# Optimization experiments

Measured on AMD Instinct MI355X. Metric: run time of the kernel, lower is better.

## Reference

```python
import jax, jax.numpy as jnp
import numpy as np

N = 50000      # nodes
E = 800000     # edges (before self-loops)
F_IN = 256
H = 4          # heads
C1 = 128
C2 = 64
NCLS = 50
NEG_SLOPE = 0.2


def setup_inputs() -> dict:
    key = jax.random.key(0)
    ks = jax.random.split(key, 12)
    x = jax.random.normal(ks[0], (N, F_IN), dtype=jnp.float32)
    edge_index = jax.random.randint(ks[1], (2, E), 0, N, dtype=jnp.int32)
    s1 = 1.0 / np.sqrt(F_IN)
    s2 = 1.0 / np.sqrt(H * C1)
    s3 = 1.0 / np.sqrt(H * C2)
    return {
        "x": x,
        "edge_index": edge_index,
        "W1": jax.random.normal(ks[2], (F_IN, H * C1), dtype=jnp.float32) * s1,
        "a_src1": jax.random.normal(ks[3], (H, C1), dtype=jnp.float32) * s2,
        "a_dst1": jax.random.normal(ks[4], (H, C1), dtype=jnp.float32) * s2,
        "b1": jnp.zeros((H * C1,), dtype=jnp.float32),
        "W2": jax.random.normal(ks[5], (H * C1, H * C2), dtype=jnp.float32) * s2,
        "a_src2": jax.random.normal(ks[6], (H, C2), dtype=jnp.float32) * s3,
        "a_dst2": jax.random.normal(ks[7], (H, C2), dtype=jnp.float32) * s3,
        "b2": jnp.zeros((H * C2,), dtype=jnp.float32),
        "Wf": jax.random.normal(ks[8], (H * C2, NCLS), dtype=jnp.float32) * s3,
        "bf": jnp.zeros((NCLS,), dtype=jnp.float32),
    }


def _gat_conv(x, src, dst, W, a_src, a_dst, b, heads, ch):
    # h: [N, H, C] transformed features
    h = (x @ W).reshape(N, heads, ch)
    # per-node attention halves (standard GAT decomposition, avoids per-edge d-dim gather for scores)
    asrc = jnp.sum(h * a_src[None], axis=-1)  # [N, H]
    adst = jnp.sum(h * a_dst[None], axis=-1)  # [N, H]
    e = jax.nn.leaky_relu(asrc[src] + adst[dst], NEG_SLOPE)  # [E, H]
    # softmax over edges sharing the same destination node
    m = jax.ops.segment_max(e, dst, num_segments=N)          # [N, H]
    ex = jnp.exp(e - m[dst])
    denom = jax.ops.segment_sum(ex, dst, num_segments=N)     # [N, H]
    alpha = ex / (denom[dst] + 1e-16)                        # [E, H]
    msg = h[src] * alpha[:, :, None]                         # [E, H, C]
    out = jax.ops.segment_sum(msg, dst, num_segments=N)      # [N, H, C]
    return out.reshape(N, heads * ch) + b


def reference(x, edge_index, W1, a_src1, a_dst1, b1, W2, a_src2, a_dst2, b2, Wf, bf):
    # PyG GATConv adds self-loops by default
    loops = jnp.arange(N, dtype=edge_index.dtype)
    src = jnp.concatenate([edge_index[0], loops])
    dst = jnp.concatenate([edge_index[1], loops])
    h = _gat_conv(x, src, dst, W1, a_src1, a_dst1, b1, H, C1)
    h = jax.nn.elu(h)
    # F.dropout is identity in eval mode
    h = _gat_conv(h, src, dst, W2, a_src2, a_dst2, b2, H, C2)
    h = jax.nn.elu(h)
    return h @ Wf + bf
```

## Files before the change

kernel.cpp:

```cpp
#include <hip/hip_runtime.h>
#include <hip/hip_fp16.h>
#include <cmath>

#define NN 50000
#define EE 800000
#define ET 850000
#define HH 4
#define CC1 128
#define CC2 64
#define FIN 256
#define NCLS 50

typedef _Float16 half8_t __attribute__((ext_vector_type(8)));
typedef __attribute__((ext_vector_type(4))) float floatx4;

typedef const __attribute__((address_space(1))) unsigned int* glds_gp_t;
typedef __attribute__((address_space(3))) unsigned int* glds_lp_t;
__device__ __forceinline__ void glds16(const void* g, void* l) {
    __builtin_amdgcn_global_load_lds((glds_gp_t)g, (glds_lp_t)l, 16, 0, 0);
}

#define NB_CAST 12500
#define NB_W1   512
#define NB_W2   512
#define NB_WF   64
__global__ __launch_bounds__(256) void prep_fused(
    const float* __restrict__ x, __half* __restrict__ xb,
    const float* __restrict__ W1, __half* __restrict__ W1t,
    const float* __restrict__ W2, __half* __restrict__ W2t,
    const float* __restrict__ Wf, __half* __restrict__ Wft)
{
    int b = blockIdx.x;
    if (b < NB_CAST) {
        int t = b * 256 + threadIdx.x;
        float4 v = *(const float4*)(x + 4 * (size_t)t);
        __half2 p[2];
        p[0] = __floats2half2_rn(v.x, v.y);
        p[1] = __floats2half2_rn(v.z, v.w);
        *(uint2*)(xb + 4 * (size_t)t) = *(uint2*)p;
    } else if (b < NB_CAST + NB_W1) {
        int t = (b - NB_CAST) * 256 + threadIdx.x;
        int n = t >> 8, k = t & 255;
        W1t[t] = __float2half(W1[(size_t)k * 512 + n]);
    } else if (b < NB_CAST + NB_W1 + NB_W2) {
        int t = (b - NB_CAST - NB_W1) * 256 + threadIdx.x;
        int n = t >> 9, k = t & 511;
        W2t[t] = __float2half(W2[(size_t)k * 256 + n]);
    } else {
        int t = (b - NB_CAST - NB_W1 - NB_W2) * 256 + threadIdx.x;
        int n = t >> 8, k = t & 255;
        Wft[t] = (n < NCLS) ? __float2half(Wf[(size_t)k * NCLS + n]) : __float2half(0.f);
    }
}

__global__ __launch_bounds__(256) void gemm_f16_v2(
    const __half* __restrict__ A,
    const __half* __restrict__ Bt,
    __half* __restrict__ C,
    int M, int N, int K)
{
    __shared__ __half As[128 * 32];
    __shared__ __half Bs[128 * 32];
    int tid = threadIdx.x, wave = tid >> 6, lane = tid & 63;
    int wm = (wave >> 1) * 64, wn = (wave & 1) * 64;
    int row0 = blockIdx.x * 128, col0 = blockIdx.y * 128;
    int lm = lane & 15, lq = lane >> 4, kq = lq * 8;
    floatx4 acc[4][4] = {};

    int srow = wave * 32 + (lane >> 2);
    int skk  = (lane & 3) * 8;
    int gra0 = row0 + srow;      if (gra0 >= M) gra0 = M - 1;
    int gra1 = row0 + srow + 16; if (gra1 >= M) gra1 = M - 1;
    const __half* ga0 = A + (size_t)gra0 * K + skk;
    const __half* ga1 = A + (size_t)gra1 * K + skk;
    const __half* gb0 = Bt + (size_t)(col0 + srow) * K + skk;
    const __half* gb1 = Bt + (size_t)(col0 + srow + 16) * K + skk;
    __half* la0 = &As[(wave * 32) * 32];
    __half* la1 = &As[(wave * 32 + 16) * 32];
    __half* lb0 = &Bs[(wave * 32) * 32];
    __half* lb1 = &Bs[(wave * 32 + 16) * 32];

    for (int k0 = 0; k0 < K; k0 += 32) {
        __syncthreads();
        glds16(ga0 + k0, la0);
        glds16(ga1 + k0, la1);
        glds16(gb0 + k0, lb0);
        glds16(gb1 + k0, lb1);
        __syncthreads();

        half8_t af[4], bfr[4];
        #pragma unroll
        for (int mt = 0; mt < 4; ++mt)
            af[mt] = *(const half8_t*)&As[(wm + mt * 16 + lm) * 32 + kq];
        #pragma unroll
        for (int nt = 0; nt < 4; ++nt)
            bfr[nt] = *(const half8_t*)&Bs[(wn + nt * 16 + lm) * 32 + kq];
        #pragma unroll
        for (int mt = 0; mt < 4; ++mt)
            #pragma unroll
            for (int nt = 0; nt < 4; ++nt)
                acc[mt][nt] = __builtin_amdgcn_mfma_f32_16x16x32_f16(
                    af[mt], bfr[nt], acc[mt][nt], 0, 0, 0);
    }

    #pragma unroll
    for (int mt = 0; mt < 4; ++mt) {
        int rbase = row0 + wm + mt * 16 + lq * 4;
        #pragma unroll
        for (int nt = 0; nt < 4; ++nt) {
            int c = col0 + wn + nt * 16 + lm;
            #pragma unroll
            for (int r = 0; r < 4; ++r) {
                int gr = rbase + r;
                if (gr < M) C[(size_t)gr * N + c] = __float2half(acc[mt][nt][r]);
            }
        }
    }
}

__global__ __launch_bounds__(128) void gemm_final(
    const __half* __restrict__ A,
    const __half* __restrict__ Bt,
    const float* __restrict__ bias,
    float* __restrict__ out, int M)
{
    __shared__ __half As[128 * 40];
    __shared__ __half Bs[64 * 40];
    int tid = threadIdx.x, wave = tid >> 6, lane = tid & 63;
    int row0 = blockIdx.x * 128;
    int lm = lane & 15, lq = lane >> 4, kq = lq * 8;
    floatx4 acc[4][4] = {};

    for (int k0 = 0; k0 < 256; k0 += 32) {
        int gr = row0 + tid; if (gr >= M) gr = M - 1;
        const __half* ap = A + (size_t)gr * 256 + k0;
        half8_t a0 = *(const half8_t*)ap;
        half8_t a1 = *(const half8_t*)(ap + 8);
        half8_t a2 = *(const half8_t*)(ap + 16);
        half8_t a3 = *(const half8_t*)(ap + 24);
        const __half* bp = Bt + (size_t)(tid >> 1) * 256 + k0 + (tid & 1) * 16;
        half8_t b0 = *(const half8_t*)bp;
        half8_t b1 = *(const half8_t*)(bp + 8);
        __syncthreads();
        *(half8_t*)&As[tid * 40 + 0]  = a0;
        *(half8_t*)&As[tid * 40 + 8]  = a1;
        *(half8_t*)&As[tid * 40 + 16] = a2;
        *(half8_t*)&As[tid * 40 + 24] = a3;
        *(half8_t*)&Bs[(tid >> 1) * 40 + (tid & 1) * 16]     = b0;
        *(half8_t*)&Bs[(tid >> 1) * 40 + (tid & 1) * 16 + 8] = b1;
        __syncthreads();

        half8_t af[4], bfr[4];
        #pragma unroll
        for (int mt = 0; mt < 4; ++mt)
            af[mt] = *(const half8_t*)&As[(wave * 64 + mt * 16 + lm) * 40 + kq];
        #pragma unroll
        for (int nt = 0; nt < 4; ++nt)
            bfr[nt] = *(const half8_t*)&Bs[(nt * 16 + lm) * 40 + kq];
        #pragma unroll
        for (int mt = 0; mt < 4; ++mt)
            #pragma unroll
            for (int nt = 0; nt < 4; ++nt)
                acc[mt][nt] = __builtin_amdgcn_mfma_f32_16x16x32_f16(
                    af[mt], bfr[nt], acc[mt][nt], 0, 0, 0);
    }

    #pragma unroll
    for (int mt = 0; mt < 4; ++mt) {
        int rbase = row0 + wave * 64 + mt * 16 + lq * 4;
        #pragma unroll
        for (int nt = 0; nt < 4; ++nt) {
            int c = nt * 16 + lm;
            if (c >= NCLS) continue;
            float bv = bias[c];
            #pragma unroll
            for (int r = 0; r < 4; ++r) {
                int gr = rbase + r;
                if (gr < M) out[(size_t)gr * NCLS + c] = acc[mt][nt][r] + bv;
            }
        }
    }
}

template<int C>
__global__ __launch_bounds__(256) void attn_scores2(
    const __half* __restrict__ h, const float* __restrict__ a_src,
    const float* __restrict__ a_dst, float* __restrict__ asrc,
    float* __restrict__ adst)
{
    constexpr int HC = HH * C;
    constexpr int CPL = HC / 64;
    int wave = threadIdx.x >> 6;
    int lane = threadIdx.x & 63;
    int n = blockIdx.x * 4 + wave;
    if (n >= NN) return;
    int c0 = lane * CPL;
    int head = c0 / C;
    const __half* hp = h + (size_t)n * HC + c0;
    float hv[CPL];
    if (CPL == 8) {
        union { uint4 u; __half2 h2[4]; } U;
        U.u = *(const uint4*)hp;
        #pragma unroll
        for (int k = 0; k < 4; ++k) {
            float2 f = __half22float2(U.h2[k]);
            hv[2 * k] = f.x; hv[2 * k + 1] = f.y;
        }
    } else {
        union { uint2 u; __half2 h2[2]; } U;
        U.u = *(const uint2*)hp;
        #pragma unroll
        for (int k = 0; k < 2; ++k) {
            float2 f = __half22float2(U.h2[k]);
            hv[2 * k] = f.x; hv[2 * k + 1] = f.y;
        }
    }
    float s1 = 0.f, s2 = 0.f;
    #pragma unroll
    for (int c = 0; c < CPL; ++c) {
        s1 += hv[c] * a_src[c0 + c];
        s2 += hv[c] * a_dst[c0 + c];
    }
    #pragma unroll
    for (int o = 8; o > 0; o >>= 1) {
        s1 += __shfl_xor(s1, o, 64);
        s2 += __shfl_xor(s2, o, 64);
    }
    if ((lane & 15) == 0) {
        asrc[n * HH + head] = s1;
        adst[n * HH + head] = s2;
    }
}

__global__ void edge_histogram(const int* __restrict__ ei, int* __restrict__ deg)
{
    int t = blockIdx.x * blockDim.x + threadIdx.x;
    if (t >= ET) return;
    int dst = (t < EE) ? ei[EE + t] : (t - EE);
    atomicAdd(&deg[dst], 1);
}

__global__ __launch_bounds__(256) void scan_reduce(
    const int* __restrict__ deg, int* __restrict__ partials)
{
    int i0 = blockIdx.x * 2048 + threadIdx.x * 8;
    int s = 0;
    #pragma unroll
    for (int k = 0; k < 8; ++k) { int i = i0 + k; s += (i < NN) ? deg[i] : 0; }
    #pragma unroll
    for (int o = 32; o > 0; o >>= 1) s += __shfl_xor(s, o, 64);
    __shared__ int ws[4];
    int lane = threadIdx.x & 63, wid = threadIdx.x >> 6;
    if (lane == 0) ws[wid] = s;
    __syncthreads();
    if (threadIdx.x == 0) partials[blockIdx.x] = ws[0] + ws[1] + ws[2] + ws[3];
}

#define SCAN_NB 25
__global__ __launch_bounds__(256) void scan_apply(
    const int* __restrict__ deg, const int* __restrict__ partials,
    int* __restrict__ off, int* __restrict__ pos)
{
    __shared__ int spE[SCAN_NB];
    __shared__ int ws[4];
    int lane = threadIdx.x & 63, wid = threadIdx.x >> 6;
    if (wid == 0) {
        int v = (lane < SCAN_NB) ? partials[lane] : 0;
        int s = v;
        #pragma unroll
        for (int o = 1; o < 32; o <<= 1) {
            int t = __shfl_up(s, o, 64);
            if (lane >= o) s += t;
        }
        if (lane < SCAN_NB) spE[lane] = s - v;
    }

    int i0 = blockIdx.x * 2048 + threadIdx.x * 8;
    int v[8]; int s = 0;
    #pragma unroll
    for (int k = 0; k < 8; ++k) {
        int i = i0 + k;
        v[k] = (i < NN) ? deg[i] : 0;
        s += v[k];
    }
    int sc = s;
    #pragma unroll
    for (int o = 1; o < 64; o <<= 1) {
        int t = __shfl_up(sc, o, 64);
        if (lane >= o) sc += t;
    }
    if (lane == 63) ws[wid] = sc;
    __syncthreads();
    int woff = spE[blockIdx.x];
    for (int w = 0; w < wid; ++w) woff += ws[w];
    int excl = woff + sc - s;
    #pragma unroll
    for (int k = 0; k < 8; ++k) {
        int i = i0 + k;
        if (i < NN) { off[i] = excl; pos[i] = excl; }
        excl += v[k];
    }
    if (blockIdx.x == 0 && threadIdx.x == 0) off[NN] = ET;
}

__global__ void edge_scatter(const int* __restrict__ ei,
                             int* __restrict__ pos, int* __restrict__ csr_src)
{
    int t = blockIdx.x * blockDim.x + threadIdx.x;
    if (t >= ET) return;
    int src, dst;
    if (t < EE) { src = ei[t]; dst = ei[EE + t]; }
    else        { src = t - EE; dst = t - EE; }
    int p = atomicAdd(&pos[dst], 1);
    csr_src[p] = src;
}

template<int C>
__global__ __launch_bounds__(256) void aggregate7(
    const __half* __restrict__ h, const int* __restrict__ off,
    const int* __restrict__ csr_src, const float* __restrict__ asrc,
    const float* __restrict__ adst, const float* __restrict__ bias,
    __half* __restrict__ outb)
{
    constexpr int HC = HH * C;
    constexpr int LPE = HC / 8;
    constexpr int EPW = 64 / LPE;
    constexpr int UNR = 8;
    __shared__ unsigned int exlds_all[4][64 * HH];
    int wave = threadIdx.x >> 6;
    int lane = threadIdx.x & 63;
    int n = blockIdx.x * 4 + wave;
    if (n >= NN) return;
    unsigned int* exlds = exlds_all[wave];
    int el  = (EPW == 1) ? 0 : (lane >> 5);
    int lel = (EPW == 1) ? lane : (lane & 31);
    int coff = lel * 8;
    int hl = coff / C;

    int start = off[n], end = off[n + 1];
    float4 advv = *(const float4*)(adst + (size_t)n * HH);
    float dh0 = 0.f, dh1 = 0.f, dh2 = 0.f, dh3 = 0.f;
    __half2 acc2[4] = {};

    for (int cb = start; cb < end; cb += 64) {
        int eidx = cb + lane;
        bool valid = eidx < end;
        int s_lane = csr_src[valid ? eidx : end - 1];
        float4 t = *(const float4*)(asrc + (size_t)s_lane * HH);
        float e0 = t.x + advv.x; e0 = e0 > 0.f ? e0 : 0.2f * e0;
        float e1 = t.y + advv.y; e1 = e1 > 0.f ? e1 : 0.2f * e1;
        float e2 = t.z + advv.z; e2 = e2 > 0.f ? e2 : 0.2f * e2;
        float e3 = t.w + advv.w; e3 = e3 > 0.f ? e3 : 0.2f * e3;
        float x0 = valid ? __expf(e0) : 0.f;
        float x1 = valid ? __expf(e1) : 0.f;
        float x2 = valid ? __expf(e2) : 0.f;
        float x3 = valid ? __expf(e3) : 0.f;
        dh0 += x0; dh1 += x1; dh2 += x2; dh3 += x3;
        __half2 xp[4];
        xp[0] = __float2half2_rn(x0);
        xp[1] = __float2half2_rn(x1);
        xp[2] = __float2half2_rn(x2);
        xp[3] = __float2half2_rn(x3);
        *(uint4*)&exlds[lane * 4] = *(uint4*)xp;

        int cnt = end - cb; if (cnt > 64) cnt = 64;
        int jmax = (cnt + UNR * EPW - 1) & ~(UNR * EPW - 1);
        for (int jj = 0; jj < jmax; jj += UNR * EPW) {
            int sidx[UNR]; __half2 xs[UNR];
            union { uint4 u; __half2 h2[4]; } uv[UNR];
            #pragma unroll
            for (int u = 0; u < UNR; ++u) {
                int e_lo = jj + u * EPW;
                if (EPW == 1) {
                    sidx[u] = __builtin_amdgcn_readlane(s_lane, e_lo);
                } else {
                    int sa = __builtin_amdgcn_readlane(s_lane, e_lo);
                    int sb = __builtin_amdgcn_readlane(s_lane, e_lo + 1);
                    sidx[u] = el ? sb : sa;
                }
                uv[u].u = *(const uint4*)(h + (size_t)sidx[u] * HC + coff);
                xs[u] = *(__half2*)&exlds[(e_lo + el) * 4 + hl];
            }
            #pragma unroll
            for (int u = 0; u < UNR; ++u)
                #pragma unroll
                for (int k = 0; k < 4; ++k)
                    acc2[k] = __hfma2(xs[u], uv[u].h2[k], acc2[k]);
        }
    }

    #pragma unroll
    for (int o = 32; o > 0; o >>= 1) {
        dh0 += __shfl_xor(dh0, o, 64);
        dh1 += __shfl_xor(dh1, o, 64);
        dh2 += __shfl_xor(dh2, o, 64);
        dh3 += __shfl_xor(dh3, o, 64);
    }
    float accf[8];
    #pragma unroll
    for (int k = 0; k < 4; ++k) {
        float2 f = __half22float2(acc2[k]);
        accf[2 * k] = f.x; accf[2 * k + 1] = f.y;
    }
    if (EPW == 2) {
        #pragma unroll
        for (int c = 0; c < 8; ++c)
            accf[c] += __shfl_xor(accf[c], 32, 64);
    }
    float d = (hl == 0) ? dh0 : (hl == 1) ? dh1 : (hl == 2) ? dh2 : dh3;
    float inv = 1.f / (d + 1e-16f);
    if (el == 0) {
        float4 b0 = *(const float4*)(bias + coff);
        float4 b1 = *(const float4*)(bias + coff + 4);
        float bb[8] = {b0.x, b0.y, b0.z, b0.w, b1.x, b1.y, b1.z, b1.w};
        __half2 pk[4];
        #pragma unroll
        for (int c2 = 0; c2 < 4; ++c2) {
            float ua = accf[2 * c2]     * inv + bb[2 * c2];
            float ub = accf[2 * c2 + 1] * inv + bb[2 * c2 + 1];
            ua = ua > 0.f ? ua : expm1f(ua);
            ub = ub > 0.f ? ub : expm1f(ub);
            pk[c2] = __floats2half2_rn(ua, ub);
        }
        *(uint4*)(outb + (size_t)n * HC + coff) = *(uint4*)pk;
    }
}

extern "C" void kernel_launch(void* const* d_in, const int* in_sizes, int n_in,
                              void* d_out, int out_size, void* d_ws, size_t ws_size,
                              hipStream_t stream) {
    const float* x      = (const float*)d_in[0];
    const int*   ei     = (const int*)d_in[1];
    const float* W1     = (const float*)d_in[2];
    const float* a_src1 = (const float*)d_in[3];
    const float* a_dst1 = (const float*)d_in[4];
    const float* b1     = (const float*)d_in[5];
    const float* W2     = (const float*)d_in[6];
    const float* a_src2 = (const float*)d_in[7];
    const float* a_dst2 = (const float*)d_in[8];
    const float* b2     = (const float*)d_in[9];
    const float* Wf     = (const float*)d_in[10];
    const float* bf     = (const float*)d_in[11];
    float* out = (float*)d_out;

    char* p = (char*)d_ws;
    __half* xb    = (__half*)p; p += (size_t)NN * FIN * 2;
    __half* h1b   = (__half*)p; p += (size_t)NN * HH * CC1 * 2;
    __half* out1b = (__half*)p; p += (size_t)NN * HH * CC1 * 2;
    __half* h2b   = (__half*)p; p += (size_t)NN * HH * CC2 * 2;
    __half* out2b = (__half*)p; p += (size_t)NN * HH * CC2 * 2;
    __half* W1t   = (__half*)p; p += (size_t)FIN * HH * CC1 * 2;
    __half* W2t   = (__half*)p; p += (size_t)HH * CC1 * HH * CC2 * 2;
    __half* Wft   = (__half*)p; p += (size_t)64 * HH * CC2 * 2;
    float* asrc   = (float*)p;  p += (size_t)NN * HH * 4;
    float* adst   = (float*)p;  p += (size_t)NN * HH * 4;
    int* deg      = (int*)p;    p += (size_t)NN * 4;
    int* csr_off  = (int*)p;    p += (size_t)(NN + 1) * 4 + 12;
    int* csr_pos  = (int*)p;    p += (size_t)NN * 4;
    int* csr_src  = (int*)p;    p += (size_t)ET * 4;
    int* partials = (int*)p;    p += 64 * 4;

    hipMemsetAsync(deg, 0, NN * sizeof(int), stream);

    prep_fused<<<NB_CAST + NB_W1 + NB_W2 + NB_WF, 256, 0, stream>>>(
        x, xb, W1, W1t, W2, W2t, Wf, Wft);

    edge_histogram<<<(ET + 255) / 256, 256, 0, stream>>>(ei, deg);
    scan_reduce<<<SCAN_NB, 256, 0, stream>>>(deg, partials);
    scan_apply<<<SCAN_NB, 256, 0, stream>>>(deg, partials, csr_off, csr_pos);
    edge_scatter<<<(ET + 255) / 256, 256, 0, stream>>>(ei, csr_pos, csr_src);

    gemm_f16_v2<<<dim3((NN + 127) / 128, (HH * CC1) / 128), 256, 0, stream>>>(
        xb, W1t, h1b, NN, HH * CC1, FIN);
    attn_scores2<CC1><<<(NN + 3) / 4, 256, 0, stream>>>(h1b, a_src1, a_dst1, asrc, adst);
    aggregate7<CC1><<<(NN + 3) / 4, 256, 0, stream>>>(h1b, csr_off, csr_src, asrc, adst, b1, out1b);

    gemm_f16_v2<<<dim3((NN + 127) / 128, (HH * CC2) / 128), 256, 0, stream>>>(
        out1b, W2t, h2b, NN, HH * CC2, HH * CC1);
    attn_scores2<CC2><<<(NN + 3) / 4, 256, 0, stream>>>(h2b, a_src2, a_dst2, asrc, adst);
    aggregate7<CC2><<<(NN + 3) / 4, 256, 0, stream>>>(h2b, csr_off, csr_src, asrc, adst, b2, out2b);

    gemm_final<<<(NN + 127) / 128, 128, 0, stream>>>(out2b, Wft, bf, out, NN);
}
```

Before: 498.5 us.

## Fuse histogram into prep kernel, merge scan passes, grid-stride attention/aggregate

```diff
diff --git a/kernel.cpp b/kernel.cpp
--- a/kernel.cpp
+++ b/kernel.cpp
@@ -24,11 +24,13 @@
 #define NB_W1   512
 #define NB_W2   512
 #define NB_WF   64
-__global__ __launch_bounds__(256) void prep_fused(
+#define NB_HIST 3321
+__global__ __launch_bounds__(256) void prep_hist(
     const float* __restrict__ x, __half* __restrict__ xb,
     const float* __restrict__ W1, __half* __restrict__ W1t,
     const float* __restrict__ W2, __half* __restrict__ W2t,
-    const float* __restrict__ Wf, __half* __restrict__ Wft)
+    const float* __restrict__ Wf, __half* __restrict__ Wft,
+    const int* __restrict__ ei, int* __restrict__ deg)
 {
     int b = blockIdx.x;
     if (b < NB_CAST) {
@@ -46,10 +48,16 @@
         int t = (b - NB_CAST - NB_W1) * 256 + threadIdx.x;
         int n = t >> 9, k = t & 511;
         W2t[t] = __float2half(W2[(size_t)k * 256 + n]);
-    } else {
+    } else if (b < NB_CAST + NB_W1 + NB_W2 + NB_WF) {
         int t = (b - NB_CAST - NB_W1 - NB_W2) * 256 + threadIdx.x;
         int n = t >> 8, k = t & 255;
         Wft[t] = (n < NCLS) ? __float2half(Wf[(size_t)k * NCLS + n]) : __float2half(0.f);
+    } else {
+        int t = (b - NB_CAST - NB_W1 - NB_W2 - NB_WF) * 256 + threadIdx.x;
+        if (t < ET) {
+            int dst = (t < EE) ? ei[EE + t] : (t - EE);
+            atomicAdd(&deg[dst], 1);
+        }
     }
 }
 
@@ -183,99 +191,79 @@
 }
 
 template<int C>
-__global__ __launch_bounds__(256) void attn_scores2(
+__global__ __launch_bounds__(256) void attn_scores3(
     const __half* __restrict__ h, const float* __restrict__ a_src,
     const float* __restrict__ a_dst, float* __restrict__ asrc,
-    float* __restrict__ adst)
+    float* __restrict__ adst, int nwaves)
 {
     constexpr int HC = HH * C;
     constexpr int CPL = HC / 64;
     int wave = threadIdx.x >> 6;
     int lane = threadIdx.x & 63;
-    int n = blockIdx.x * 4 + wave;
-    if (n >= NN) return;
+    int wid0 = blockIdx.x * 4 + wave;
     int c0 = lane * CPL;
     int head = c0 / C;
-    const __half* hp = h + (size_t)n * HC + c0;
-    float hv[CPL];
-    if (CPL == 8) {
-        union { uint4 u; __half2 h2[4]; } U;
-        U.u = *(const uint4*)hp;
-        #pragma unroll
-        for (int k = 0; k < 4; ++k) {
-            float2 f = __half22float2(U.h2[k]);
-            hv[2 * k] = f.x; hv[2 * k + 1] = f.y;
-        }
-    } else {
-        union { uint2 u; __half2 h2[2]; } U;
-        U.u = *(const uint2*)hp;
-        #pragma unroll
-        for (int k = 0; k < 2; ++k) {
-            float2 f = __half22float2(U.h2[k]);
-            hv[2 * k] = f.x; hv[2 * k + 1] = f.y;
-        }
-    }
-    float s1 = 0.f, s2 = 0.f;
-    #pragma unroll
-    for (int c = 0; c < CPL; ++c) {
-        s1 += hv[c] * a_src[c0 + c];
-        s2 += hv[c] * a_dst[c0 + c];
-    }
-    #pragma unroll
-    for (int o = 8; o > 0; o >>= 1) {
-        s1 += __shfl_xor(s1, o, 64);
-        s2 += __shfl_xor(s2, o, 64);
-    }
-    if ((lane & 15) == 0) {
-        asrc[n * HH + head] = s1;
-        adst[n * HH + head] = s2;
-    }
-}
-
-__global__ void edge_histogram(const int* __restrict__ ei, int* __restrict__ deg)
-{
-    int t = blockIdx.x * blockDim.x + threadIdx.x;
-    if (t >= ET) return;
-    int dst = (t < EE) ? ei[EE + t] : (t - EE);
-    atomicAdd(&deg[dst], 1);
-}
-
-__global__ __launch_bounds__(256) void scan_reduce(
-    const int* __restrict__ deg, int* __restrict__ partials)
-{
-    int i0 = blockIdx.x * 2048 + threadIdx.x * 8;
-    int s = 0;
-    #pragma unroll
-    for (int k = 0; k < 8; ++k) { int i = i0 + k; s += (i < NN) ? deg[i] : 0; }
-    #pragma unroll
-    for (int o = 32; o > 0; o >>= 1) s += __shfl_xor(s, o, 64);
+
+    for (int n = wid0; n < NN; n += nwaves) {
+        const __half* hp = h + (size_t)n * HC + c0;
+        float hv[CPL];
+        if (CPL == 8) {
+            union { uint4 u; __half2 h2[4]; } U;
+            U.u = *(const uint4*)hp;
+            #pragma unroll
+            for (int k = 0; k < 4; ++k) {
+                float2 f = __half22float2(U.h2[k]);
+                hv[2 * k] = f.x; hv[2 * k + 1] = f.y;
+            }
+        } else {
+            union { uint2 u; __half2 h2[2]; } U;
+            U.u = *(const uint2*)hp;
+            #pragma unroll
+            for (int k = 0; k < 2; ++k) {
+                float2 f = __half22float2(U.h2[k]);
+                hv[2 * k] = f.x; hv[2 * k + 1] = f.y;
+            }
+        }
+        float s1 = 0.f, s2 = 0.f;
+        #pragma unroll
+        for (int c = 0; c < CPL; ++c) {
+            s1 += hv[c] * a_src[c0 + c];
+            s2 += hv[c] * a_dst[c0 + c];
+        }
+        #pragma unroll
+        for (int o = 8; o > 0; o >>= 1) {
+            s1 += __shfl_xor(s1, o, 64);
+            s2 += __shfl_xor(s2, o, 64);
+        }
+        if ((lane & 15) == 0) {
+            asrc[n * HH + head] = s1;
+            adst[n * HH + head] = s2;
+        }
+    }
+}
+
+#define SCAN_NB 25
+__global__ __launch_bounds__(256) void scan_fused(
+    const int* __restrict__ deg, int* __restrict__ off, int* __restrict__ pos)
+{
     __shared__ int ws[4];
-    int lane = threadIdx.x & 63, wid = threadIdx.x >> 6;
-    if (lane == 0) ws[wid] = s;
+    __shared__ int base_s;
+    int tid = threadIdx.x;
+    int lane = tid & 63, wid = tid >> 6;
+
+    int lim = blockIdx.x * 2048;
+    int s0 = 0;
+    for (int i = tid; i < lim; i += 256) s0 += deg[i];
+    #pragma unroll
+    for (int o = 32; o > 0; o >>= 1) s0 += __shfl_xor(s0, o, 64);
+    if (lane == 0) ws[wid] = s0;
     __syncthreads();
-    if (threadIdx.x == 0) partials[blockIdx.x] = ws[0] + ws[1] + ws[2] + ws[3];
-}
-
-#define SCAN_NB 25
-__global__ __launch_bounds__(256) void scan_apply(
-    const int* __restrict__ deg, const int* __restrict__ partials,
-    int* __restrict__ off, int* __restrict__ pos)
-{
-    __shared__ int spE[SCAN_NB];
-    __shared__ int ws[4];
-    int lane = threadIdx.x & 63, wid = threadIdx.x >> 6;
-    if (wid == 0) {
-        int v = (lane < SCAN_NB) ? partials[lane] : 0;
-        int s = v;
-        #pragma unroll
-        for (int o = 1; o < 32; o <<= 1) {
-            int t = __shfl_up(s, o, 64);
-            if (lane >= o) s += t;
-        }
-        if (lane < SCAN_NB) spE[lane] = s - v;
-    }
-
-    int i0 = blockIdx.x * 2048 + threadIdx.x * 8;
+    if (tid == 0) base_s = ws[0] + ws[1] + ws[2] + ws[3];
+    __syncthreads();
+    int base = base_s;
+    __syncthreads();
+
+    int i0 = blockIdx.x * 2048 + tid * 8;
     int v[8]; int s = 0;
     #pragma unroll
     for (int k = 0; k < 8; ++k) {
@@ -291,7 +279,7 @@
     }
     if (lane == 63) ws[wid] = sc;
     __syncthreads();
-    int woff = spE[blockIdx.x];
+    int woff = base;
     for (int w = 0; w < wid; ++w) woff += ws[w];
     int excl = woff + sc - s;
     #pragma unroll
@@ -300,7 +288,7 @@
         if (i < NN) { off[i] = excl; pos[i] = excl; }
         excl += v[k];
     }
-    if (blockIdx.x == 0 && threadIdx.x == 0) off[NN] = ET;
+    if (blockIdx.x == 0 && tid == 0) off[NN] = ET;
 }
 
 __global__ void edge_scatter(const int* __restrict__ ei,
@@ -316,11 +304,11 @@
 }
 
 template<int C>
-__global__ __launch_bounds__(256) void aggregate7(
+__global__ __launch_bounds__(256) void aggregate8(
     const __half* __restrict__ h, const int* __restrict__ off,
     const int* __restrict__ csr_src, const float* __restrict__ asrc,
     const float* __restrict__ adst, const float* __restrict__ bias,
-    __half* __restrict__ outb)
+    __half* __restrict__ outb, int nwaves)
 {
     constexpr int HC = HH * C;
     constexpr int LPE = HC / 8;
@@ -329,100 +317,101 @@
     __shared__ unsigned int exlds_all[4][64 * HH];
     int wave = threadIdx.x >> 6;
     int lane = threadIdx.x & 63;
-    int n = blockIdx.x * 4 + wave;
-    if (n >= NN) return;
+    int wid0 = blockIdx.x * 4 + wave;
     unsigned int* exlds = exlds_all[wave];
     int el  = (EPW == 1) ? 0 : (lane >> 5);
     int lel = (EPW == 1) ? lane : (lane & 31);
     int coff = lel * 8;
     int hl = coff / C;
 
-    int start = off[n], end = off[n + 1];
-    float4 advv = *(const float4*)(adst + (size_t)n * HH);
-    float dh0 = 0.f, dh1 = 0.f, dh2 = 0.f, dh3 = 0.f;
-    __half2 acc2[4] = {};
-
-    for (int cb = start; cb < end; cb += 64) {
-        int eidx = cb + lane;
-        bool valid = eidx < end;
-        int s_lane = csr_src[valid ? eidx : end - 1];
-        float4 t = *(const float4*)(asrc + (size_t)s_lane * HH);
-        float e0 = t.x + advv.x; e0 = e0 > 0.f ? e0 : 0.2f * e0;
-        float e1 = t.y + advv.y; e1 = e1 > 0.f ? e1 : 0.2f * e1;
-        float e2 = t.z + advv.z; e2 = e2 > 0.f ? e2 : 0.2f * e2;
-        float e3 = t.w + advv.w; e3 = e3 > 0.f ? e3 : 0.2f * e3;
-        float x0 = valid ? __expf(e0) : 0.f;
-        float x1 = valid ? __expf(e1) : 0.f;
-        float x2 = valid ? __expf(e2) : 0.f;
-        float x3 = valid ? __expf(e3) : 0.f;
-        dh0 += x0; dh1 += x1; dh2 += x2; dh3 += x3;
-        __half2 xp[4];
-        xp[0] = __float2half2_rn(x0);
-        xp[1] = __float2half2_rn(x1);
-        xp[2] = __float2half2_rn(x2);
-        xp[3] = __float2half2_rn(x3);
-        *(uint4*)&exlds[lane * 4] = *(uint4*)xp;
-
-        int cnt = end - cb; if (cnt > 64) cnt = 64;
-        int jmax = (cnt + UNR * EPW - 1) & ~(UNR * EPW - 1);
-        for (int jj = 0; jj < jmax; jj += UNR * EPW) {
-            int sidx[UNR]; __half2 xs[UNR];
-            union { uint4 u; __half2 h2[4]; } uv[UNR];
-            #pragma unroll
-            for (int u = 0; u < UNR; ++u) {
-                int e_lo = jj + u * EPW;
-                if (EPW == 1) {
-                    sidx[u] = __builtin_amdgcn_readlane(s_lane, e_lo);
-                } else {
-                    int sa = __builtin_amdgcn_readlane(s_lane, e_lo);
-                    int sb = __builtin_amdgcn_readlane(s_lane, e_lo + 1);
-                    sidx[u] = el ? sb : sa;
+    for (int n = wid0; n < NN; n += nwaves) {
+        int start = off[n], end = off[n + 1];
+        float4 advv = *(const float4*)(adst + (size_t)n * HH);
+        float dh0 = 0.f, dh1 = 0.f, dh2 = 0.f, dh3 = 0.f;
+        __half2 acc2[4] = {};
+
+        for (int cb = start; cb < end; cb += 64) {
+            int eidx = cb + lane;
+            bool valid = eidx < end;
+            int s_lane = csr_src[valid ? eidx : end - 1];
+            float4 t = *(const float4*)(asrc + (size_t)s_lane * HH);
+            float e0 = t.x + advv.x; e0 = e0 > 0.f ? e0 : 0.2f * e0;
+            float e1 = t.y + advv.y; e1 = e1 > 0.f ? e1 : 0.2f * e1;
+            float e2 = t.z + advv.z; e2 = e2 > 0.f ? e2 : 0.2f * e2;
+            float e3 = t.w + advv.w; e3 = e3 > 0.f ? e3 : 0.2f * e3;
+            float x0 = valid ? __expf(e0) : 0.f;
+            float x1 = valid ? __expf(e1) : 0.f;
+            float x2 = valid ? __expf(e2) : 0.f;
+            float x3 = valid ? __expf(e3) : 0.f;
+            dh0 += x0; dh1 += x1; dh2 += x2; dh3 += x3;
+            __half2 xp[4];
+            xp[0] = __float2half2_rn(x0);
+            xp[1] = __float2half2_rn(x1);
+            xp[2] = __float2half2_rn(x2);
+            xp[3] = __float2half2_rn(x3);
+            *(uint4*)&exlds[lane * 4] = *(uint4*)xp;
+
+            int cnt = end - cb; if (cnt > 64) cnt = 64;
+            int jmax = (cnt + UNR * EPW - 1) & ~(UNR * EPW - 1);
+            for (int jj = 0; jj < jmax; jj += UNR * EPW) {
+                int sidx[UNR]; __half2 xs[UNR];
+                union { uint4 u; __half2 h2[4]; } uv[UNR];
+                #pragma unroll
+                for (int u = 0; u < UNR; ++u) {
+                    int e_lo = jj + u * EPW;
+                    if (EPW == 1) {
+                        sidx[u] = __builtin_amdgcn_readlane(s_lane, e_lo);
+                    } else {
+                        int sa = __builtin_amdgcn_readlane(s_lane, e_lo);
+                        int sb = __builtin_amdgcn_readlane(s_lane, e_lo + 1);
+                        sidx[u] = el ? sb : sa;
+                    }
+                    uv[u].u = *(const uint4*)(h + (size_t)sidx[u] * HC + coff);
+                    xs[u] = *(__half2*)&exlds[(e_lo + el) * 4 + hl];
                 }
-                uv[u].u = *(const uint4*)(h + (size_t)sidx[u] * HC + coff);
-                xs[u] = *(__half2*)&exlds[(e_lo + el) * 4 + hl];
-            }
-            #pragma unroll
-            for (int u = 0; u < UNR; ++u)
                 #pragma unroll
-                for (int k = 0; k < 4; ++k)
-                    acc2[k] = __hfma2(xs[u], uv[u].h2[k], acc2[k]);
-        }
-    }
-
-    #pragma unroll
-    for (int o = 32; o > 0; o >>= 1) {
-        dh0 += __shfl_xor(dh0, o, 64);
-        dh1 += __shfl_xor(dh1, o, 64);
-        dh2 += __shfl_xor(dh2, o, 64);
-        dh3 += __shfl_xor(dh3, o, 64);
-    }
-    float accf[8];
-    #pragma unroll
-    for (int k = 0; k < 4; ++k) {
-        float2 f = __half22float2(acc2[k]);
-        accf[2 * k] = f.x; accf[2 * k + 1] = f.y;
-    }
-    if (EPW == 2) {
-        #pragma unroll
-        for (int c = 0; c < 8; ++c)
-            accf[c] += __shfl_xor(accf[c], 32, 64);
-    }
-    float d = (hl == 0) ? dh0 : (hl == 1) ? dh1 : (hl == 2) ? dh2 : dh3;
-    float inv = 1.f / (d + 1e-16f);
-    if (el == 0) {
-        float4 b0 = *(const float4*)(bias + coff);
-        float4 b1 = *(const float4*)(bias + coff + 4);
-        float bb[8] = {b0.x, b0.y, b0.z, b0.w, b1.x, b1.y, b1.z, b1.w};
-        __half2 pk[4];
-        #pragma unroll
-        for (int c2 = 0; c2 < 4; ++c2) {
-            float ua = accf[2 * c2]     * inv + bb[2 * c2];
-            float ub = accf[2 * c2 + 1] * inv + bb[2 * c2 + 1];
-            ua = ua > 0.f ? ua : expm1f(ua);
-            ub = ub > 0.f ? ub : expm1f(ub);
-            pk[c2] = __floats2half2_rn(ua, ub);
-        }
-        *(uint4*)(outb + (size_t)n * HC + coff) = *(uint4*)pk;
+                for (int u = 0; u < UNR; ++u)
+                    #pragma unroll
+                    for (int k = 0; k < 4; ++k)
+                        acc2[k] = __hfma2(xs[u], uv[u].h2[k], acc2[k]);
+            }
+        }
+
+        #pragma unroll
+        for (int o = 32; o > 0; o >>= 1) {
+            dh0 += __shfl_xor(dh0, o, 64);
+            dh1 += __shfl_xor(dh1, o, 64);
+            dh2 += __shfl_xor(dh2, o, 64);
+            dh3 += __shfl_xor(dh3, o, 64);
+        }
+        float accf[8];
+        #pragma unroll
+        for (int k = 0; k < 4; ++k) {
+            float2 f = __half22float2(acc2[k]);
+            accf[2 * k] = f.x; accf[2 * k + 1] = f.y;
+        }
+        if (EPW == 2) {
+            #pragma unroll
+            for (int c = 0; c < 8; ++c)
+                accf[c] += __shfl_xor(accf[c], 32, 64);
+        }
+        float d = (hl == 0) ? dh0 : (hl == 1) ? dh1 : (hl == 2) ? dh2 : dh3;
+        float inv = 1.f / (d + 1e-16f);
+        if (el == 0) {
+            float4 b0 = *(const float4*)(bias + coff);
+            float4 b1 = *(const float4*)(bias + coff + 4);
+            float bb[8] = {b0.x, b0.y, b0.z, b0.w, b1.x, b1.y, b1.z, b1.w};
+            __half2 pk[4];
+            #pragma unroll
+            for (int c2 = 0; c2 < 4; ++c2) {
+                float ua = accf[2 * c2]     * inv + bb[2 * c2];
+                float ub = accf[2 * c2 + 1] * inv + bb[2 * c2 + 1];
+                ua = ua > 0.f ? ua : expm1f(ua);
+                ub = ub > 0.f ? ub : expm1f(ub);
+                pk[c2] = __floats2half2_rn(ua, ub);
+            }
+            *(uint4*)(outb + (size_t)n * HC + coff) = *(uint4*)pk;
+        }
     }
 }
 
@@ -458,27 +447,29 @@
     int* csr_off  = (int*)p;    p += (size_t)(NN + 1) * 4 + 12;
     int* csr_pos  = (int*)p;    p += (size_t)NN * 4;
     int* csr_src  = (int*)p;    p += (size_t)ET * 4;
-    int* partials = (int*)p;    p += 64 * 4;
 
     hipMemsetAsync(deg, 0, NN * sizeof(int), stream);
 
-    prep_fused<<<NB_CAST + NB_W1 + NB_W2 + NB_WF, 256, 0, stream>>>(
-        x, xb, W1, W1t, W2, W2t, Wf, Wft);
-
-    edge_histogram<<<(ET + 255) / 256, 256, 0, stream>>>(ei, deg);
-    scan_reduce<<<SCAN_NB, 256, 0, stream>>>(deg, partials);
-    scan_apply<<<SCAN_NB, 256, 0, stream>>>(deg, partials, csr_off, csr_pos);
+    prep_hist<<<NB_CAST + NB_W1 + NB_W2 + NB_WF + NB_HIST, 256, 0, stream>>>(
+        x, xb, W1, W1t, W2, W2t, Wf, Wft, ei, deg);
+
+    scan_fused<<<SCAN_NB, 256, 0, stream>>>(deg, csr_off, csr_pos);
     edge_scatter<<<(ET + 255) / 256, 256, 0, stream>>>(ei, csr_pos, csr_src);
+
+    const int AGG_NB = 2048;
+    const int AGG_NW = AGG_NB * 4;
+    const int ATT_NB = 2048;
+    const int ATT_NW = ATT_NB * 4;
 
     gemm_f16_v2<<<dim3((NN + 127) / 128, (HH * CC1) / 128), 256, 0, stream>>>(
         xb, W1t, h1b, NN, HH * CC1, FIN);
-    attn_scores2<CC1><<<(NN + 3) / 4, 256, 0, stream>>>(h1b, a_src1, a_dst1, asrc, adst);
-    aggregate7<CC1><<<(NN + 3) / 4, 256, 0, stream>>>(h1b, csr_off, csr_src, asrc, adst, b1, out1b);
+    attn_scores3<CC1><<<ATT_NB, 256, 0, stream>>>(h1b, a_src1, a_dst1, asrc, adst, ATT_NW);
+    aggregate8<CC1><<<AGG_NB, 256, 0, stream>>>(h1b, csr_off, csr_src, asrc, adst, b1, out1b, AGG_NW);
 
     gemm_f16_v2<<<dim3((NN + 127) / 128, (HH * CC2) / 128), 256, 0, stream>>>(
         out1b, W2t, h2b, NN, HH * CC2, HH * CC1);
-    attn_scores2<CC2><<<(NN + 3) / 4, 256, 0, stream>>>(h2b, a_src2, a_dst2, asrc, adst);
-    aggregate7<CC2><<<(NN + 3) / 4, 256, 0, stream>>>(h2b, csr_off, csr_src, asrc, adst, b2, out2b);
+    attn_scores3<CC2><<<ATT_NB, 256, 0, stream>>>(h2b, a_src2, a_dst2, asrc, adst, ATT_NW);
+    aggregate8<CC2><<<AGG_NB, 256, 0, stream>>>(h2b, csr_off, csr_src, asrc, adst, b2, out2b, AGG_NW);
 
     gemm_final<<<(NN + 127) / 128, 128, 0, stream>>>(out2b, Wft, bf, out, NN);
 }
```

Measured after the change: 530.4 us. 1.06x slower.
